# Optimization experiments

Hardware: AMD Instinct MI355X
Metric: run time of the kernel (lower is better)

## Reference

```python
import jax, jax.numpy as jnp
import numpy as np

B, S, D_MODEL = 4, 2048, 1024
N_HEAD, D_K, D_V = 16, 64, 64
LN_EPS = 1e-5


def setup_inputs() -> dict:
    key = jax.random.key(0)
    ks = jax.random.split(key, 8)
    std_qk = np.sqrt(2.0 / (D_MODEL + D_K)).astype(np.float32)
    std_v = np.sqrt(2.0 / (D_MODEL + D_V)).astype(np.float32)
    return {
        "q": jax.random.normal(ks[0], (B, S, D_MODEL), dtype=jnp.float32),
        "k": jax.random.normal(ks[1], (B, S, D_MODEL), dtype=jnp.float32),
        "v": jax.random.normal(ks[2], (B, S, D_MODEL), dtype=jnp.float32),
        "attn_mask": jax.random.randint(ks[3], (B, 1, S), 0, 2) > 0,
        # torch Linear weights: (out_features, in_features)
        "w_q": jax.random.normal(ks[4], (N_HEAD * D_K, D_MODEL), dtype=jnp.float32) * std_qk,
        "w_k": jax.random.normal(ks[5], (N_HEAD * D_K, D_MODEL), dtype=jnp.float32) * std_qk,
        "w_v": jax.random.normal(ks[6], (N_HEAD * D_V, D_MODEL), dtype=jnp.float32) * std_v,
        "w_fc": jax.random.normal(ks[7], (D_MODEL, N_HEAD * D_V), dtype=jnp.float32) * np.sqrt(2.0 / (D_MODEL + N_HEAD * D_V)).astype(np.float32),
        "ln_gamma": jnp.ones((D_MODEL,), dtype=jnp.float32),
        "ln_beta": jnp.zeros((D_MODEL,), dtype=jnp.float32),
    }


def _layer_norm(x, gamma, beta):
    mu = jnp.mean(x, axis=-1, keepdims=True)
    var = jnp.mean(jnp.square(x - mu), axis=-1, keepdims=True)
    return (x - mu) * jax.lax.rsqrt(var + LN_EPS) * gamma + beta


def reference(q, k, v, attn_mask, w_q, w_k, w_v, w_fc, ln_gamma, ln_beta):
    b, sq, _ = q.shape
    residual = q
    qh = (q @ w_q.T).reshape(b, sq, N_HEAD, D_K)          # [b,sq,h,dk]
    kh = (k @ w_k.T).reshape(b, -1, N_HEAD, D_K)          # [b,sk,h,dk]
    vh = (v @ w_v.T).reshape(b, -1, N_HEAD, D_V)          # [b,sk,h,dv]
    temperature = jnp.asarray(np.power(D_K, 0.5), dtype=q.dtype)
    scores = jnp.einsum("bqhd,bkhd->bhqk", qh, kh) / temperature
    # attn_mask: [b,1,sk] key-padding mask, True = masked
    scores = jnp.where(attn_mask[:, None, :, :], jnp.asarray(-1e6, scores.dtype), scores)
    attn = jax.nn.softmax(scores, axis=-1)                 # dropout is identity in eval
    out = jnp.einsum("bhqk,bkhd->bqhd", attn, vh).reshape(b, sq, N_HEAD * D_V)
    out = out @ w_fc.T
    out = _layer_norm(out + residual, ln_gamma, ln_beta)
    return out, attn
```

## Files before the change

### kernel.cpp

```cpp
#include <hip/hip_runtime.h>
#include <cstdint>
#include <cstddef>
#include <cmath>

#define B_  4
#define S_  2048
#define DM_ 1024
#define H_  16

typedef _Float16 h8 __attribute__((ext_vector_type(8)));
typedef _Float16 h4 __attribute__((ext_vector_type(4)));
typedef float f32x4 __attribute__((ext_vector_type(4)));

#define MFMA16(A_, B2_, C_) __builtin_amdgcn_mfma_f32_16x16x32_f16((A_), (B2_), (C_), 0, 0, 0)

#define C_EXP2 0.18033688011112042f
#define BIAS2_UNMASKED -14.426950408889634f
#define BIAS2_MASKED   -60000.0f

__device__ __forceinline__ void gload_lds16(const void* g, void* l) {
  __builtin_amdgcn_global_load_lds(
      (const __attribute__((address_space(1))) unsigned int*)g,
      (__attribute__((address_space(3))) unsigned int*)l, 16, 0, 0);
}

__global__ __launch_bounds__(256) void cvt_kernel(const float* __restrict__ in,
                                                  _Float16* __restrict__ out, int n4) {
  int i = blockIdx.x * 256 + threadIdx.x;
  if (i < n4) {
    f32x4 v = ((const f32x4*)in)[i];
    h4 o;
    o[0] = (_Float16)v[0]; o[1] = (_Float16)v[1];
    o[2] = (_Float16)v[2]; o[3] = (_Float16)v[3];
    ((h4*)out)[i] = o;
  }
}

template <int MODE, int A16>
__global__ __launch_bounds__(256, 2)
void gemm_bt(const void* __restrict__ Ap, const void* __restrict__ Wp,
             void* __restrict__ outp, int M, int N, int K) {
  __shared__ _Float16 As[128 * 32];
  __shared__ _Float16 Bs[128 * 32];
  const int tid = threadIdx.x;
  const int w = tid >> 6, lane = tid & 63;
  const int g = lane >> 4, li = lane & 15;
  const int wr = w >> 1, wc = w & 1;
  const int mBase = blockIdx.y * 128, nBase = blockIdx.x * 128;

  f32x4 acc[4][4] = {};

  _Float16* lA = As + w * 1024;
  _Float16* lB = Bs + w * 1024;

  const _Float16* gA16 =
      (const _Float16*)Ap + (size_t)(mBase + w * 32 + (lane >> 2)) * K + (lane & 3) * 8;
  const float* gA32 =
      (const float*)Ap + (size_t)(mBase + w * 32 + (lane >> 3)) * K + (lane & 7) * 4;
  const float* gW =
      (const float*)Wp + (size_t)(nBase + w * 32 + (lane >> 3)) * K + (lane & 7) * 4;

  for (int kt = 0; kt < K; kt += 32) {
    if (kt) __syncthreads();
    if constexpr (A16) {
      gload_lds16(gA16 + kt, lA);
      gload_lds16(gA16 + kt + (size_t)16 * K, lA + 512);
    } else {
#pragma unroll
      for (int it = 0; it < 4; ++it) {
        f32x4 v = *(const f32x4*)(gA32 + kt + (size_t)(it * 8) * K);
        h4 o;
        o[0] = (_Float16)v[0]; o[1] = (_Float16)v[1];
        o[2] = (_Float16)v[2]; o[3] = (_Float16)v[3];
        *(h4*)&lA[(it * 8 + (lane >> 3)) * 32 + (lane & 7) * 4] = o;
      }
    }
#pragma unroll
    for (int it = 0; it < 4; ++it) {
      f32x4 v = *(const f32x4*)(gW + kt + (size_t)(it * 8) * K);
      h4 o;
      o[0] = (_Float16)v[0]; o[1] = (_Float16)v[1];
      o[2] = (_Float16)v[2]; o[3] = (_Float16)v[3];
      *(h4*)&lB[(it * 8 + (lane >> 3)) * 32 + (lane & 7) * 4] = o;
    }
    __syncthreads();
    h8 af[4], bf[4];
#pragma unroll
    for (int t = 0; t < 4; ++t) af[t] = *(const h8*)&As[(wr * 64 + t * 16 + li) * 32 + g * 8];
#pragma unroll
    for (int u = 0; u < 4; ++u) bf[u] = *(const h8*)&Bs[(wc * 64 + u * 16 + li) * 32 + g * 8];
#pragma unroll
    for (int t = 0; t < 4; ++t)
#pragma unroll
      for (int u = 0; u < 4; ++u) acc[t][u] = MFMA16(af[t], bf[u], acc[t][u]);
  }

#pragma unroll
  for (int t = 0; t < 4; ++t) {
    const int grow0 = mBase + wr * 64 + t * 16 + g * 4;
#pragma unroll
    for (int u = 0; u < 4; ++u) {
      const int gcol = nBase + wc * 64 + u * 16 + li;
      if (MODE == 2) {
        float* o = (float*)outp;
#pragma unroll
        for (int r = 0; r < 4; ++r) o[(size_t)(grow0 + r) * N + gcol] = acc[t][u][r];
      } else if (MODE == 0) {
        _Float16* o = (_Float16*)outp;
        const int hh = gcol >> 6, d = gcol & 63;
#pragma unroll
        for (int r = 0; r < 4; ++r) {
          const int grow = grow0 + r;
          const int bb = grow >> 11, ss = grow & 2047;
          o[((size_t)((bb * H_ + hh) * S_ + ss)) * 64 + d] = (_Float16)acc[t][u][r];
        }
      } else {
        _Float16* o = (_Float16*)outp;
        const int hh = gcol >> 6, d = gcol & 63;
        const int bb = grow0 >> 11, ss = grow0 & 2047;
        h4 vv;
#pragma unroll
        for (int r = 0; r < 4; ++r) vv[r] = (_Float16)acc[t][u][r];
        *(h4*)&o[((size_t)((bb * H_ + hh) * 64 + d)) * S_ + ss] = vv;
      }
    }
  }
}

__global__ __launch_bounds__(256, 6)
void qk1_kernel(const _Float16* __restrict__ qh, const _Float16* __restrict__ kh,
                const int* __restrict__ mask, float* __restrict__ rlws) {
  __shared__ _Float16 sbias[S_];
  __shared__ __align__(16) _Float16 Ks[128 * 72];
  const int tid = threadIdx.x;
  const int w = tid >> 6, lane = tid & 63;
  const int g = lane >> 4, li = lane & 15;
  const int id = blockIdx.x;
  const int hh = id & 15, bb = (id >> 4) & 3, qt = id >> 6;
  const size_t bhS = ((size_t)bb * H_ + hh) * S_;
  const _Float16* khb = kh + bhS * 64;

  {
    const int4* mi = (const int4*)(mask + (size_t)bb * S_);
    int4 m0 = mi[tid * 2];
    int4 m1 = mi[tid * 2 + 1];
    _Float16* d = sbias + tid * 8;
    d[0] = m0.x ? (_Float16)BIAS2_MASKED : (_Float16)BIAS2_UNMASKED;
    d[1] = m0.y ? (_Float16)BIAS2_MASKED : (_Float16)BIAS2_UNMASKED;
    d[2] = m0.z ? (_Float16)BIAS2_MASKED : (_Float16)BIAS2_UNMASKED;
    d[3] = m0.w ? (_Float16)BIAS2_MASKED : (_Float16)BIAS2_UNMASKED;
    d[4] = m1.x ? (_Float16)BIAS2_MASKED : (_Float16)BIAS2_UNMASKED;
    d[5] = m1.y ? (_Float16)BIAS2_MASKED : (_Float16)BIAS2_UNMASKED;
    d[6] = m1.z ? (_Float16)BIAS2_MASKED : (_Float16)BIAS2_UNMASKED;
    d[7] = m1.w ? (_Float16)BIAS2_MASKED : (_Float16)BIAS2_UNMASKED;
  }

  h8 aq[2][2];
#pragma unroll
  for (int t = 0; t < 2; ++t) {
    const _Float16* qp = qh + (bhS + qt * 128 + w * 32 + t * 16 + li) * 64;
    aq[t][0] = *(const h8*)(qp + g * 8);
    aq[t][1] = *(const h8*)(qp + 32 + g * 8);
  }

  const int srow = tid >> 3;
  const int ssl = tid & 7;

  float l[2][4] = {};
  for (int kc = 0; kc < 16; ++kc) {
    __syncthreads();
#pragma unroll
    for (int rnd = 0; rnd < 4; ++rnd) {
      const int row = rnd * 32 + srow;
      const h8 kv = *(const h8*)(khb + (size_t)(kc * 128 + row) * 64 + ssl * 8);
      *(h8*)&Ks[row * 72 + ssl * 8] = kv;
    }
    __syncthreads();
    for (int kk = 0; kk < 8; ++kk) {
      const int krow = kk * 16 + li;
      const h8 bk0 = *(const h8*)&Ks[krow * 72 + g * 8];
      const h8 bk1 = *(const h8*)&Ks[krow * 72 + 32 + g * 8];
      const float bias = (float)sbias[kc * 128 + krow];
#pragma unroll
      for (int t = 0; t < 2; ++t) {
        f32x4 a = {0.f, 0.f, 0.f, 0.f};
        a = MFMA16(aq[t][0], bk0, a);
        a = MFMA16(aq[t][1], bk1, a);
#pragma unroll
        for (int r = 0; r < 4; ++r) l[t][r] += exp2f(fmaf(a[r], C_EXP2, bias));
      }
    }
  }

#pragma unroll
  for (int t = 0; t < 2; ++t)
#pragma unroll
    for (int r = 0; r < 4; ++r) {
      float s = l[t][r];
      s += __shfl_xor(s, 1);
      s += __shfl_xor(s, 2);
      s += __shfl_xor(s, 4);
      s += __shfl_xor(s, 8);
      if (li == 0)
        rlws[bhS + qt * 128 + w * 32 + t * 16 + g * 4 + r] = 1.0f / s;
    }
}

__global__ __launch_bounds__(256, 4)
void qk2_kernel(const _Float16* __restrict__ qh, const _Float16* __restrict__ kh,
                const _Float16* __restrict__ vt, const int* __restrict__ mask,
                const float* __restrict__ rlws, float* __restrict__ attn_out,
                _Float16* __restrict__ ctx) {
  __shared__ _Float16 sbias[S_];
  __shared__ __align__(16) _Float16 Ks[64 * 72];
  __shared__ __align__(16) _Float16 Vs[64 * 72];
  __shared__ __align__(16) _Float16 Pst[4][16 * 72];
  const int tid = threadIdx.x;
  const int w = tid >> 6, lane = tid & 63;
  const int g = lane >> 4, li = lane & 15;
  const int id = blockIdx.x;
  const int hh = id & 15, bb = (id >> 4) & 3, qt = id >> 6;
  const size_t bhS = ((size_t)bb * H_ + hh) * S_;
  const _Float16* khb = kh + bhS * 64;
  const _Float16* Vbg = vt + bhS * 64;

  {
    const int4* mi = (const int4*)(mask + (size_t)bb * S_);
    int4 m0 = mi[tid * 2];
    int4 m1 = mi[tid * 2 + 1];
    _Float16* d = sbias + tid * 8;
    d[0] = m0.x ? (_Float16)BIAS2_MASKED : (_Float16)BIAS2_UNMASKED;
    d[1] = m0.y ? (_Float16)BIAS2_MASKED : (_Float16)BIAS2_UNMASKED;
    d[2] = m0.z ? (_Float16)BIAS2_MASKED : (_Float16)BIAS2_UNMASKED;
    d[3] = m0.w ? (_Float16)BIAS2_MASKED : (_Float16)BIAS2_UNMASKED;
    d[4] = m1.x ? (_Float16)BIAS2_MASKED : (_Float16)BIAS2_UNMASKED;
    d[5] = m1.y ? (_Float16)BIAS2_MASKED : (_Float16)BIAS2_UNMASKED;
    d[6] = m1.z ? (_Float16)BIAS2_MASKED : (_Float16)BIAS2_UNMASKED;
    d[7] = m1.w ? (_Float16)BIAS2_MASKED : (_Float16)BIAS2_UNMASKED;
  }

  h8 aq[2][2];
  float rl[2][4];
#pragma unroll
  for (int t = 0; t < 2; ++t) {
    const _Float16* qp = qh + (bhS + qt * 128 + w * 32 + t * 16 + li) * 64;
    aq[t][0] = *(const h8*)(qp + g * 8);
    aq[t][1] = *(const h8*)(qp + 32 + g * 8);
#pragma unroll
    for (int r = 0; r < 4; ++r)
      rl[t][r] = rlws[bhS + qt * 128 + w * 32 + t * 16 + g * 4 + r];
  }

  float* ab = attn_out + (bhS + qt * 128) * S_;
  _Float16* Pw = &Pst[w][0];
  f32x4 acc[2][4] = {};

  const int srow = tid >> 3;
  const int ssl = tid & 7;
  const int strow = lane >> 4;
  const int stcol = (lane & 15) * 4;

  for (int kc = 0; kc < 32; ++kc) {
    __syncthreads();
#pragma unroll
    for (int rnd = 0; rnd < 2; ++rnd) {
      const int row = rnd * 32 + srow;
      const h8 kv = *(const h8*)(khb + (size_t)(kc * 64 + row) * 64 + ssl * 8);
      *(h8*)&Ks[row * 72 + ssl * 8] = kv;
      const h8 vv = *(const h8*)(Vbg + (size_t)row * S_ + kc * 64 + ssl * 8);
      *(h8*)&Vs[row * 72 + ssl * 8] = vv;
    }
    __syncthreads();

#pragma unroll
    for (int t = 0; t < 2; ++t) {
#pragma unroll
      for (int kk = 0; kk < 4; ++kk) {
        const int krow = kk * 16 + li;
        const h8 bk0 = *(const h8*)&Ks[krow * 72 + g * 8];
        const h8 bk1 = *(const h8*)&Ks[krow * 72 + 32 + g * 8];
        const float bias = (float)sbias[kc * 64 + krow];
        f32x4 a = {0.f, 0.f, 0.f, 0.f};
        a = MFMA16(aq[t][0], bk0, a);
        a = MFMA16(aq[t][1], bk1, a);
#pragma unroll
        for (int r = 0; r < 4; ++r)
          Pw[(g * 4 + r) * 72 + krow] =
              (_Float16)(exp2f(fmaf(a[r], C_EXP2, bias)) * rl[t][r]);
      }
#pragma unroll
      for (int rr = 0; rr < 4; ++rr) {
        const int row4 = rr * 4 + strow;
        const h4 p = *(const h4*)&Pw[row4 * 72 + stcol];
        f32x4 o;
        o[0] = (float)p[0]; o[1] = (float)p[1];
        o[2] = (float)p[2]; o[3] = (float)p[3];
        __builtin_nontemporal_store(
            o, (f32x4*)(ab + (size_t)(w * 32 + t * 16 + row4) * S_ + kc * 64 + stcol));
      }
#pragma unroll
      for (int ks = 0; ks < 2; ++ks) {
        const h8 pa = *(const h8*)&Pw[li * 72 + ks * 32 + g * 8];
#pragma unroll
        for (int u = 0; u < 4; ++u) {
          const h8 bf = *(const h8*)&Vs[(u * 16 + li) * 72 + ks * 32 + g * 8];
          acc[t][u] = MFMA16(pa, bf, acc[t][u]);
        }
      }
    }
  }

  _Float16* cb = ctx + ((size_t)bb * S_ + qt * 128 + w * 32 + g * 4) * DM_ + hh * 64 + li;
#pragma unroll
  for (int t = 0; t < 2; ++t)
#pragma unroll
    for (int u = 0; u < 4; ++u)
#pragma unroll
      for (int r = 0; r < 4; ++r)
        cb[(size_t)(t * 16 + r) * DM_ + u * 16] = (_Float16)acc[t][u][r];
}

__global__ __launch_bounds__(256)
void ln_kernel(const float* __restrict__ fc, const float* __restrict__ resid,
               const float* __restrict__ gamma, const float* __restrict__ beta,
               float* __restrict__ out) {
  __shared__ float red[8];
  const int row = blockIdx.x;
  const int t = threadIdx.x, w = t >> 6, lane = t & 63;
  const f32x4 xv = *(const f32x4*)(fc + (size_t)row * DM_ + t * 4);
  const f32x4 rv = *(const f32x4*)(resid + (size_t)row * DM_ + t * 4);
  float x0 = xv[0] + rv[0], x1 = xv[1] + rv[1], x2 = xv[2] + rv[2], x3 = xv[3] + rv[3];
  float s = x0 + x1 + x2 + x3;
#pragma unroll
  for (int off = 1; off < 64; off <<= 1) s += __shfl_xor(s, off);
  if (lane == 0) red[w] = s;
  __syncthreads();
  const float mu = (red[0] + red[1] + red[2] + red[3]) * (1.0f / (float)DM_);
  const float d0 = x0 - mu, d1 = x1 - mu, d2 = x2 - mu, d3 = x3 - mu;
  float sq = d0 * d0 + d1 * d1 + d2 * d2 + d3 * d3;
#pragma unroll
  for (int off = 1; off < 64; off <<= 1) sq += __shfl_xor(sq, off);
  if (lane == 0) red[4 + w] = sq;
  __syncthreads();
  const float inv = rsqrtf((red[4] + red[5] + red[6] + red[7]) * (1.0f / (float)DM_) + 1e-5f);
  const f32x4 gv = *(const f32x4*)(gamma + t * 4);
  const f32x4 bv = *(const f32x4*)(beta + t * 4);
  f32x4 o;
  o[0] = d0 * inv * gv[0] + bv[0];
  o[1] = d1 * inv * gv[1] + bv[1];
  o[2] = d2 * inv * gv[2] + bv[2];
  o[3] = d3 * inv * gv[3] + bv[3];
  *(f32x4*)(out + (size_t)row * DM_ + t * 4) = o;
}

extern "C" void kernel_launch(void* const* d_in, const int* in_sizes, int n_in,
                              void* d_out, int out_size, void* d_ws, size_t ws_size,
                              hipStream_t stream) {
  const float* q = (const float*)d_in[0];
  const float* k = (const float*)d_in[1];
  const float* v = (const float*)d_in[2];
  const int* mask = (const int*)d_in[3];
  const float* wq = (const float*)d_in[4];
  const float* wk = (const float*)d_in[5];
  const float* wv = (const float*)d_in[6];
  const float* wfc = (const float*)d_in[7];
  const float* gamma = (const float*)d_in[8];
  const float* beta = (const float*)d_in[9];

  float* out0 = (float*)d_out;
  float* attn = out0 + (size_t)B_ * S_ * DM_;
  float* rlws = out0;

  char* ws = (char*)d_ws;
  _Float16* qhp = (_Float16*)(ws + (0ull << 20));
  _Float16* khp = (_Float16*)(ws + (16ull << 20));
  _Float16* vtp = (_Float16*)(ws + (32ull << 20));
  _Float16* ctxp = (_Float16*)(ws + (48ull << 20));
  float* fcp = (float*)(ws + (0ull << 20));
  _Float16* stg = (_Float16*)(ws + (48ull << 20));

  const int nqkv4 = B_ * S_ * DM_ / 4;
  dim3 gg(DM_ / 128, B_ * S_ / 128);

  cvt_kernel<<<nqkv4 / 256, 256, 0, stream>>>(q, stg, nqkv4);
  gemm_bt<0, 1><<<gg, 256, 0, stream>>>(stg, wq, qhp, B_ * S_, DM_, DM_);
  cvt_kernel<<<nqkv4 / 256, 256, 0, stream>>>(k, stg, nqkv4);
  gemm_bt<0, 1><<<gg, 256, 0, stream>>>(stg, wk, khp, B_ * S_, DM_, DM_);
  cvt_kernel<<<nqkv4 / 256, 256, 0, stream>>>(v, stg, nqkv4);
  gemm_bt<1, 1><<<gg, 256, 0, stream>>>(stg, wv, vtp, B_ * S_, DM_, DM_);

  qk1_kernel<<<dim3(1024), 256, 0, stream>>>(qhp, khp, mask, rlws);
  qk2_kernel<<<dim3(1024), 256, 0, stream>>>(qhp, khp, vtp, mask, rlws, attn, ctxp);

  gemm_bt<2, 1><<<gg, 256, 0, stream>>>(ctxp, wfc, fcp, B_ * S_, DM_, DM_);

  ln_kernel<<<B_ * S_, 256, 0, stream>>>(fcp, q, gamma, beta, out0);
}
```

Measured before the change: 576.4 us.

## Fuse two-pass attention kernels and drop fp32-to-fp16 conversion passes

Merges the row-sum pass (qk1) and the probability/context pass (qk2) into a single kernel. The normalizers now stay in registers instead of going through a workspace round trip, which saves one launch and the reload of Q. It also removes the three separate cvt_kernel passes by having the projection GEMMs read fp32 inputs directly (A16=0). The fused kernel uses 64-row K tiles and occupancy 4 in the first pass, where qk1 ran at occupancy 6, and the GEMMs now load fp32 A tiles, which doubles the A-operand traffic per tile.

After: 503.6 us. -12.6%, faster.

```diff
diff --git a/kernel.cpp b/kernel.cpp
--- a/kernel.cpp
+++ b/kernel.cpp
@@ -22,18 +22,6 @@
   __builtin_amdgcn_global_load_lds(
       (const __attribute__((address_space(1))) unsigned int*)g,
       (__attribute__((address_space(3))) unsigned int*)l, 16, 0, 0);
-}
-
-__global__ __launch_bounds__(256) void cvt_kernel(const float* __restrict__ in,
-                                                  _Float16* __restrict__ out, int n4) {
-  int i = blockIdx.x * 256 + threadIdx.x;
-  if (i < n4) {
-    f32x4 v = ((const f32x4*)in)[i];
-    h4 o;
-    o[0] = (_Float16)v[0]; o[1] = (_Float16)v[1];
-    o[2] = (_Float16)v[2]; o[3] = (_Float16)v[3];
-    ((h4*)out)[i] = o;
-  }
 }
 
 template <int MODE, int A16>
@@ -127,11 +115,14 @@
   }
 }
 
-__global__ __launch_bounds__(256, 6)
-void qk1_kernel(const _Float16* __restrict__ qh, const _Float16* __restrict__ kh,
-                const int* __restrict__ mask, float* __restrict__ rlws) {
+__global__ __launch_bounds__(256, 4)
+void attn_kernel(const _Float16* __restrict__ qh, const _Float16* __restrict__ kh,
+                 const _Float16* __restrict__ vt, const int* __restrict__ mask,
+                 float* __restrict__ attn_out, _Float16* __restrict__ ctx) {
   __shared__ _Float16 sbias[S_];
-  __shared__ __align__(16) _Float16 Ks[128 * 72];
+  __shared__ __align__(16) _Float16 Ks[64 * 72];
+  __shared__ __align__(16) _Float16 Vs[64 * 72];
+  __shared__ __align__(16) _Float16 Pst[4][16 * 72];
   const int tid = threadIdx.x;
   const int w = tid >> 6, lane = tid & 63;
   const int g = lane >> 4, li = lane & 15;
@@ -139,6 +130,7 @@
   const int hh = id & 15, bb = (id >> 4) & 3, qt = id >> 6;
   const size_t bhS = ((size_t)bb * H_ + hh) * S_;
   const _Float16* khb = kh + bhS * 64;
+  const _Float16* Vbg = vt + bhS * 64;
 
   {
     const int4* mi = (const int4*)(mask + (size_t)bb * S_);
@@ -167,20 +159,21 @@
   const int ssl = tid & 7;
 
   float l[2][4] = {};
-  for (int kc = 0; kc < 16; ++kc) {
-    __syncthreads();
-#pragma unroll
-    for (int rnd = 0; rnd < 4; ++rnd) {
+  for (int kc = 0; kc < 32; ++kc) {
+    __syncthreads();
+#pragma unroll
+    for (int rnd = 0; rnd < 2; ++rnd) {
       const int row = rnd * 32 + srow;
-      const h8 kv = *(const h8*)(khb + (size_t)(kc * 128 + row) * 64 + ssl * 8);
+      const h8 kv = *(const h8*)(khb + (size_t)(kc * 64 + row) * 64 + ssl * 8);
       *(h8*)&Ks[row * 72 + ssl * 8] = kv;
     }
     __syncthreads();
-    for (int kk = 0; kk < 8; ++kk) {
+#pragma unroll
+    for (int kk = 0; kk < 4; ++kk) {
       const int krow = kk * 16 + li;
       const h8 bk0 = *(const h8*)&Ks[krow * 72 + g * 8];
       const h8 bk1 = *(const h8*)&Ks[krow * 72 + 32 + g * 8];
-      const float bias = (float)sbias[kc * 128 + krow];
+      const float bias = (float)sbias[kc * 64 + krow];
 #pragma unroll
       for (int t = 0; t < 2; ++t) {
         f32x4 a = {0.f, 0.f, 0.f, 0.f};
@@ -192,6 +185,7 @@
     }
   }
 
+  float rl[2][4];
 #pragma unroll
   for (int t = 0; t < 2; ++t)
 #pragma unroll
@@ -201,62 +195,12 @@
       s += __shfl_xor(s, 2);
       s += __shfl_xor(s, 4);
       s += __shfl_xor(s, 8);
-      if (li == 0)
-        rlws[bhS + qt * 128 + w * 32 + t * 16 + g * 4 + r] = 1.0f / s;
-    }
-}
-
-__global__ __launch_bounds__(256, 4)
-void qk2_kernel(const _Float16* __restrict__ qh, const _Float16* __restrict__ kh,
-                const _Float16* __restrict__ vt, const int* __restrict__ mask,
-                const float* __restrict__ rlws, float* __restrict__ attn_out,
-                _Float16* __restrict__ ctx) {
-  __shared__ _Float16 sbias[S_];
-  __shared__ __align__(16) _Float16 Ks[64 * 72];
-  __shared__ __align__(16) _Float16 Vs[64 * 72];
-  __shared__ __align__(16) _Float16 Pst[4][16 * 72];
-  const int tid = threadIdx.x;
-  const int w = tid >> 6, lane = tid & 63;
-  const int g = lane >> 4, li = lane & 15;
-  const int id = blockIdx.x;
-  const int hh = id & 15, bb = (id >> 4) & 3, qt = id >> 6;
-  const size_t bhS = ((size_t)bb * H_ + hh) * S_;
-  const _Float16* khb = kh + bhS * 64;
-  const _Float16* Vbg = vt + bhS * 64;
-
-  {
-    const int4* mi = (const int4*)(mask + (size_t)bb * S_);
-    int4 m0 = mi[tid * 2];
-    int4 m1 = mi[tid * 2 + 1];
-    _Float16* d = sbias + tid * 8;
-    d[0] = m0.x ? (_Float16)BIAS2_MASKED : (_Float16)BIAS2_UNMASKED;
-    d[1] = m0.y ? (_Float16)BIAS2_MASKED : (_Float16)BIAS2_UNMASKED;
-    d[2] = m0.z ? (_Float16)BIAS2_MASKED : (_Float16)BIAS2_UNMASKED;
-    d[3] = m0.w ? (_Float16)BIAS2_MASKED : (_Float16)BIAS2_UNMASKED;
-    d[4] = m1.x ? (_Float16)BIAS2_MASKED : (_Float16)BIAS2_UNMASKED;
-    d[5] = m1.y ? (_Float16)BIAS2_MASKED : (_Float16)BIAS2_UNMASKED;
-    d[6] = m1.z ? (_Float16)BIAS2_MASKED : (_Float16)BIAS2_UNMASKED;
-    d[7] = m1.w ? (_Float16)BIAS2_MASKED : (_Float16)BIAS2_UNMASKED;
-  }
-
-  h8 aq[2][2];
-  float rl[2][4];
-#pragma unroll
-  for (int t = 0; t < 2; ++t) {
-    const _Float16* qp = qh + (bhS + qt * 128 + w * 32 + t * 16 + li) * 64;
-    aq[t][0] = *(const h8*)(qp + g * 8);
-    aq[t][1] = *(const h8*)(qp + 32 + g * 8);
-#pragma unroll
-    for (int r = 0; r < 4; ++r)
-      rl[t][r] = rlws[bhS + qt * 128 + w * 32 + t * 16 + g * 4 + r];
-  }
+      rl[t][r] = 1.0f / s;
+    }
 
   float* ab = attn_out + (bhS + qt * 128) * S_;
   _Float16* Pw = &Pst[w][0];
   f32x4 acc[2][4] = {};
-
-  const int srow = tid >> 3;
-  const int ssl = tid & 7;
   const int strow = lane >> 4;
   const int stcol = (lane & 15) * 4;
 
@@ -369,7 +313,6 @@
 
   float* out0 = (float*)d_out;
   float* attn = out0 + (size_t)B_ * S_ * DM_;
-  float* rlws = out0;
 
   char* ws = (char*)d_ws;
   _Float16* qhp = (_Float16*)(ws + (0ull << 20));
@@ -377,20 +320,13 @@
   _Float16* vtp = (_Float16*)(ws + (32ull << 20));
   _Float16* ctxp = (_Float16*)(ws + (48ull << 20));
   float* fcp = (float*)(ws + (0ull << 20));
-  _Float16* stg = (_Float16*)(ws + (48ull << 20));
-
-  const int nqkv4 = B_ * S_ * DM_ / 4;
+
   dim3 gg(DM_ / 128, B_ * S_ / 128);
-
-  cvt_kernel<<<nqkv4 / 256, 256, 0, stream>>>(q, stg, nqkv4);
-  gemm_bt<0, 1><<<gg, 256, 0, stream>>>(stg, wq, qhp, B_ * S_, DM_, DM_);
-  cvt_kernel<<<nqkv4 / 256, 256, 0, stream>>>(k, stg, nqkv4);
-  gemm_bt<0, 1><<<gg, 256, 0, stream>>>(stg, wk, khp, B_ * S_, DM_, DM_);
-  cvt_kernel<<<nqkv4 / 256, 256, 0, stream>>>(v, stg, nqkv4);
-  gemm_bt<1, 1><<<gg, 256, 0, stream>>>(stg, wv, vtp, B_ * S_, DM_, DM_);
-
-  qk1_kernel<<<dim3(1024), 256, 0, stream>>>(qhp, khp, mask, rlws);
-  qk2_kernel<<<dim3(1024), 256, 0, stream>>>(qhp, khp, vtp, mask, rlws, attn, ctxp);
+  gemm_bt<0, 0><<<gg, 256, 0, stream>>>(q, wq, qhp, B_ * S_, DM_, DM_);
+  gemm_bt<0, 0><<<gg, 256, 0, stream>>>(k, wk, khp, B_ * S_, DM_, DM_);
+  gemm_bt<1, 0><<<gg, 256, 0, stream>>>(v, wv, vtp, B_ * S_, DM_, DM_);
+
+  attn_kernel<<<dim3(1024), 256, 0, stream>>>(qhp, khp, vtp, mask, attn, ctxp);
 
   gemm_bt<2, 1><<<gg, 256, 0, stream>>>(ctxp, wfc, fcp, B_ * S_, DM_, DM_);
 
```
